# Kernel optimization log

Hardware: AMD Instinct MI355X
Metric: run time of the kernel (lower is better)

## Reference

```python
import jax, jax.numpy as jnp
import numpy as np

KH, KW, F = 2, 3, 32  # ConvLSTM kernel and filters


def _conv(x, w, padding):
    # x: [B,H,W,Cin], w: [kh,kw,Cin,Cout]
    return jax.lax.conv_general_dilated(
        x, w, (1, 1), padding, dimension_numbers=("NHWC", "HWIO", "NHWC"))


def _hard_sigmoid(x):
    # Keras hard_sigmoid: clip(0.2*x + 0.5, 0, 1)
    return jnp.clip(0.2 * x + 0.5, 0.0, 1.0)


def convlstm2d(x, W, U, b):
    # Keras ConvLSTM2D, padding='valid' on input conv, 'same' on recurrent conv,
    # activation=relu, recurrent_activation=hard_sigmoid, return_sequences=True.
    B, T, H, Wd, C = x.shape
    f = W.shape[-1] // 4
    Ho, Wo = H - KH + 1, Wd - KW + 1
    h0 = jnp.zeros((B, Ho, Wo, f), x.dtype)

    def step(carry, xt):
        h, c = carry
        z = _conv(xt, W, "VALID") + _conv(h, U, "SAME") + b
        zi, zf, zc, zo = jnp.split(z, 4, axis=-1)  # gate order i,f,c,o
        i = _hard_sigmoid(zi)
        fg = _hard_sigmoid(zf)
        c_new = fg * c + i * jax.nn.relu(zc)
        h_new = _hard_sigmoid(zo) * jax.nn.relu(c_new)
        return (h_new, c_new), h_new

    xs = jnp.moveaxis(x, 1, 0)  # [T,B,H,W,C]
    _, hs = jax.lax.scan(step, (h0, h0), xs)
    return jnp.moveaxis(hs, 0, 1)  # [B,T,Ho,Wo,F]


def maxpool3d(x):
    # MaxPooling3D pool_size=(1,2,2) over (T,H,W) of [B,T,H,W,C]
    return jax.lax.reduce_window(x, -jnp.inf, jax.lax.max,
                                 (1, 1, 2, 2, 1), (1, 1, 2, 2, 1), "VALID")


def setup_inputs() -> dict:
    key = jax.random.key(0)
    ks = jax.random.split(key, 12)
    s = 0.05
    B, T, H, Wd, C = 16, 12, 48, 48, 3
    x = jax.random.normal(ks[0], (B, T, H, Wd, C), jnp.float32)
    W1 = jax.random.normal(ks[1], (KH, KW, C, 4 * F), jnp.float32) * s
    U1 = jax.random.normal(ks[2], (KH, KW, F, 4 * F), jnp.float32) * s
    b1 = jnp.zeros((4 * F,), jnp.float32)
    W2 = jax.random.normal(ks[3], (KH, KW, F, 4 * F), jnp.float32) * s
    U2 = jax.random.normal(ks[4], (KH, KW, F, 4 * F), jnp.float32) * s
    b2 = jnp.zeros((4 * F,), jnp.float32)
    # after two convlstms: 48->47->46 (H), 48->46->44 (W); pool -> 23x22
    flat = T * 23 * 22 * F  # 194304
    Wd1 = jax.random.normal(ks[5], (flat, 10), jnp.float32) * 0.01
    bd1 = jnp.zeros((10,), jnp.float32)
    Wd2 = jax.random.normal(ks[6], (10, 1), jnp.float32) * 0.1
    bd2 = jnp.zeros((1,), jnp.float32)
    return {"x": x, "W1": W1, "U1": U1, "b1": b1, "W2": W2, "U2": U2,
            "b2": b2, "Wd1": Wd1, "bd1": bd1, "Wd2": Wd2, "bd2": bd2}


def reference(x, W1, U1, b1, W2, U2, b2, Wd1, bd1, Wd2, bd2):
    h1 = convlstm2d(x, W1, U1, b1)
    h2 = convlstm2d(h1, W2, U2, b2)
    p = maxpool3d(h2)            # dropout = identity at inference
    f = p.reshape(p.shape[0], -1)
    d1 = f @ Wd1 + bd1
    return d1 @ Wd2 + bd2        # [B,1]
```

## Files before the change

kernel.cpp:

```cpp
#include <hip/hip_runtime.h>
#include <math.h>

#define NB 16
#define TT 12
#define H1 47
#define W1D 46
#define H2 46
#define W2D 44

typedef short short8v __attribute__((ext_vector_type(8)));
typedef float floatx4 __attribute__((ext_vector_type(4)));

__device__ __forceinline__ short f2bf(float x) {
    unsigned u = __float_as_uint(x);
    u = (u + 0x7FFFu + ((u >> 16) & 1u)) >> 16;
    return (short)u;
}
__device__ __forceinline__ float bf2f(short s) {
    return __uint_as_float(((unsigned)(unsigned short)s) << 16);
}
__device__ __forceinline__ float hsig(float z) {
    return fminf(fmaxf(0.2f * z + 0.5f, 0.f), 1.f);
}

__global__ __launch_bounds__(256) void convert_x(const float* __restrict__ x,
                                                 short* __restrict__ xbf, int n) {
    int i = blockIdx.x * 256 + threadIdx.x;
    if (i < n) xbf[i] = f2bf(x[i]);
}

__global__ __launch_bounds__(256) void transform_w(
    const float* __restrict__ W1s, const float* __restrict__ U1s,
    const float* __restrict__ W2s, const float* __restrict__ U2s,
    short* __restrict__ Bt1, short* __restrict__ Bt2)
{
    int idx = blockIdx.x * 256 + threadIdx.x;
    int layer2 = idx >= 28672;
    int i = layer2 ? idx - 28672 : idx;
    int ci = i & 31, j = (i >> 5) & 15, g = (i >> 9) & 3, fh = (i >> 11) & 1, c = i >> 12;
    int col = g * 32 + fh * 16 + j;
    float v = 0.f;
    if (!layer2) {
        if (c == 0) {
            if (ci < 18) { int kk = ci / 3, cc = ci - kk * 3; v = W1s[(kk * 3 + cc) * 128 + col]; }
        } else {
            v = U1s[((c - 1) * 32 + ci) * 128 + col];
        }
    } else {
        if (c < 6) v = W2s[(c * 32 + ci) * 128 + col];
        else       v = U2s[((c - 6) * 32 + ci) * 128 + col];
    }
    (layer2 ? Bt2 : Bt1)[i] = f2bf(v);
}

template<int LAYER>
__device__ __forceinline__ void step_body(
    const short* __restrict__ xin,
    const short* __restrict__ hprev,
    const short* __restrict__ Bt,
    const float* __restrict__ bias,
    float* __restrict__ cstp,
    short* __restrict__ hnext,
    short* __restrict__ pool, int t2, int t1,
    int b, int y0, int x0, short* ldsrec, short* ldsaux)
{
    constexpr int Ho   = (LAYER == 1) ? H1 : H2;
    constexpr int Wo   = (LAYER == 1) ? W1D : W2D;
    constexpr int NCH  = (LAYER == 1) ? 7 : 12;
    constexpr int REC0 = (LAYER == 1) ? 1 : 6;
    constexpr int IBS  = (LAYER == 1) ? (TT * 48 * 48 * 3) : (H1 * W1D * 32);
    constexpr int HBS  = Ho * Wo * 32;

    const int tid = threadIdx.x;
    const int lane = tid & 63;
    const int fh = tid >> 6;
    const int tx = lane & 15, q = lane >> 4;
    const short8v z8 = (short8v)0;

    {
        const short* hb0 = hprev + b * HBS;
        for (int i = tid; i < 360; i += 128) {
            int p = i >> 2, c4 = i & 3;
            int row = p / 18, col = p - row * 18;
            int y = y0 + row, x = x0 + col - 1;
            short8v v = z8;
            if (y < Ho && (unsigned)x < (unsigned)Wo)
                v = *(const short8v*)(hb0 + (y * Wo + x) * 32 + c4 * 8);
            *(short8v*)&ldsrec[p * 40 + c4 * 8] = v;
        }
    }

    if (LAYER == 1) {
        const short* xb0 = xin + b * IBS + t1 * 6912;
        for (int i = tid; i < 64 * 32; i += 128) {
            int m = i >> 5, k = i & 31;
            short v = 0;
            if (k < 18) {
                int kk = k / 3, cc = k - kk * 3;
                int ky = (kk >= 3) ? 1 : 0, kx = kk - ky * 3;
                int ys = y0 + (m >> 4) + ky; if (ys > 47) ys = 47;
                int xs = x0 + (m & 15) + kx; if (xs > 47) xs = 47;
                v = xb0[(ys * 48 + xs) * 3 + cc];
            }
            ldsaux[m * 40 + k] = v;
        }
    } else {
        const short* ib0 = xin + b * IBS;
        for (int i = tid; i < 360; i += 128) {
            int p = i >> 2, c4 = i & 3;
            int row = p / 18, col = p - row * 18;
            int ys = y0 + row; if (ys > H1 - 1) ys = H1 - 1;
            int xs = x0 + col;
            short8v v = *(const short8v*)(ib0 + (ys * W1D + xs) * 32 + c4 * 8);
            *(short8v*)&ldsaux[p * 40 + c4 * 8] = v;
        }
    }
    __syncthreads();

    const short* Btl = Bt + fh * 2048 + tx * 32 + q * 8;
    floatx4 acc[4][4] = {};

#pragma unroll
    for (int c = 0; c < NCH; ++c) {
        short8v bf4[4], af[4];
#pragma unroll
        for (int g = 0; g < 4; ++g)
            bf4[g] = *(const short8v*)(Btl + c * 4096 + g * 512);

        if (LAYER == 1 && c == 0) {
#pragma unroll
            for (int a = 0; a < 4; ++a)
                af[a] = *(const short8v*)&ldsaux[(a * 16 + tx) * 40 + q * 8];
        } else if (LAYER == 2 && c < REC0) {
            int ky = (c >= 3) ? 1 : 0, kx = c - ky * 3;
#pragma unroll
            for (int a = 0; a < 4; ++a)
                af[a] = *(const short8v*)&ldsaux[(((a + ky) * 18 + tx + kx)) * 40 + q * 8];
        } else {
            int kk = c - REC0;
            int ky = (kk >= 3) ? 1 : 0, kx = kk - ky * 3;
#pragma unroll
            for (int a = 0; a < 4; ++a)
                af[a] = *(const short8v*)&ldsrec[(((a + ky) * 18 + tx + kx)) * 40 + q * 8];
        }
#pragma unroll
        for (int a = 0; a < 4; ++a)
#pragma unroll
            for (int g = 0; g < 4; ++g)
                acc[a][g] = __builtin_amdgcn_mfma_f32_16x16x32_bf16(af[a], bf4[g], acc[a][g], 0, 0, 0);
    }

    const int f = fh * 16 + tx;
    const float bi = bias[f], bfv = bias[32 + f], bcv = bias[64 + f], bov = bias[96 + f];
    float* cme = cstp + tid * 16;
    float hv[4][4];
#pragma unroll
    for (int a = 0; a < 4; ++a) {
        int y = y0 + a;
        bool yok = y < Ho;
        floatx4 cold = *(floatx4*)(cme + a * 4);
        floatx4 cnew;
#pragma unroll
        for (int r = 0; r < 4; ++r) {
            int xe = x0 + q * 4 + r;
            float ig = hsig(acc[a][0][r] + bi);
            float fg = hsig(acc[a][1][r] + bfv);
            float gg = fmaxf(acc[a][2][r] + bcv, 0.f);
            float og = hsig(acc[a][3][r] + bov);
            float cn = fg * cold[r] + ig * gg;
            cnew[r] = cn;
            float hn = 0.f;
            if (yok && xe < Wo) {
                short hb = f2bf(og * fmaxf(cn, 0.f));
                hnext[b * HBS + (y * Wo + xe) * 32 + f] = hb;
                hn = bf2f(hb);
            }
            hv[a][r] = hn;
        }
        *(floatx4*)(cme + a * 4) = cnew;
    }

    if (LAYER == 2) {
#pragma unroll
        for (int ap = 0; ap < 2; ++ap) {
            int py = y0 / 2 + ap;
#pragma unroll
            for (int rp = 0; rp < 2; ++rp) {
                int px = x0 / 2 + q * 2 + rp;
                if (py < 23 && px < 22) {
                    float m = fmaxf(fmaxf(hv[2 * ap][2 * rp],     hv[2 * ap][2 * rp + 1]),
                                    fmaxf(hv[2 * ap + 1][2 * rp], hv[2 * ap + 1][2 * rp + 1]));
                    pool[(size_t)b * 194304 + ((t2 * 23 + py) * 22 + px) * 32 + f] = f2bf(m);
                }
            }
        }
    }
}

__global__ __launch_bounds__(128) void fused_step(
    const short* __restrict__ xbf,
    const short* __restrict__ h1r, short* __restrict__ h1w,
    const short* __restrict__ h2r, short* __restrict__ h2w,
    const short* __restrict__ Bt1, const short* __restrict__ Bt2,
    const float* __restrict__ b1, const float* __restrict__ b2,
    float* __restrict__ c1, float* __restrict__ c2,
    short* __restrict__ pool, int t2, int t1, int do1, int do2)
{
    __shared__ short lds[7200];
    int gid  = blockIdx.x;
    int layer = gid & 1;
    int b     = (gid >> 1) & 15;
    int t36   = gid >> 5;
    int y0 = (t36 / 3) * 4;
    int x0 = (t36 % 3) * 16;

    if (layer == 0) {
        if (!do1) return;
        float* cstp = c1 + (size_t)(b * 36 + t36) * 2048;
        step_body<1>(xbf, h1r, Bt1, b1, cstp, h1w, nullptr, 0, t1,
                     b, y0, x0, lds, lds + 3600);
    } else {
        if (!do2) return;
        float* cstp = c2 + (size_t)(b * 36 + t36) * 2048;
        step_body<2>(h1r, h2r, Bt2, b2, cstp, h2w, pool, t2, 0,
                     b, y0, x0, lds, lds + 3600);
    }
}

__global__ __launch_bounds__(256) void gemv_kernel(
    const short* __restrict__ p, const float* __restrict__ Wd1, float* __restrict__ d1)
{
    int by = blockIdx.y;
    int k0 = blockIdx.x * 3036;
    float part[4][10];
#pragma unroll
    for (int bb = 0; bb < 4; bb++)
#pragma unroll
        for (int j = 0; j < 10; j++) part[bb][j] = 0.f;

    for (int k = k0 + threadIdx.x; k < k0 + 3036; k += 256) {
        const float* wr = Wd1 + (size_t)k * 10;
        float wv[10];
#pragma unroll
        for (int j = 0; j < 10; j++) wv[j] = wr[j];
#pragma unroll
        for (int bb = 0; bb < 4; bb++) {
            float m = bf2f(p[(size_t)(by * 4 + bb) * 194304 + k]);
#pragma unroll
            for (int j = 0; j < 10; j++) part[bb][j] = fmaf(m, wv[j], part[bb][j]);
        }
    }
    __shared__ float red[4][10][4];
    int lane = threadIdx.x & 63, wv2 = threadIdx.x >> 6;
#pragma unroll
    for (int bb = 0; bb < 4; bb++)
#pragma unroll
        for (int j = 0; j < 10; j++) {
            float v = part[bb][j];
            for (int off = 32; off > 0; off >>= 1) v += __shfl_down(v, off);
            if (lane == 0) red[bb][j][wv2] = v;
        }
    __syncthreads();
    if (threadIdx.x < 40) {
        int bb = threadIdx.x / 10, j = threadIdx.x % 10;
        float s = red[bb][j][0] + red[bb][j][1] + red[bb][j][2] + red[bb][j][3];
        atomicAdd(&d1[(by * 4 + bb) * 10 + j], s);
    }
}

__global__ void final_dense(const float* __restrict__ d1, const float* __restrict__ bd1,
                            const float* __restrict__ Wd2, const float* __restrict__ bd2,
                            float* __restrict__ out)
{
    int b = threadIdx.x;
    if (b < NB) {
        float s = bd2[0];
#pragma unroll
        for (int j = 0; j < 10; j++) s += (d1[b * 10 + j] + bd1[j]) * Wd2[j];
        out[b] = s;
    }
}

extern "C" void kernel_launch(void* const* d_in, const int* in_sizes, int n_in,
                              void* d_out, int out_size, void* d_ws, size_t ws_size,
                              hipStream_t stream)
{
    const float* x   = (const float*)d_in[0];
    const float* W1s = (const float*)d_in[1];
    const float* U1s = (const float*)d_in[2];
    const float* b1  = (const float*)d_in[3];
    const float* W2s = (const float*)d_in[4];
    const float* U2s = (const float*)d_in[5];
    const float* b2  = (const float*)d_in[6];
    const float* Wd1 = (const float*)d_in[7];
    const float* bd1 = (const float*)d_in[8];
    const float* Wd2 = (const float*)d_in[9];
    const float* bd2 = (const float*)d_in[10];
    float* out = (float*)d_out;

    const int H1N = NB * H1 * W1D * 32;
    const int H2N = NB * H2 * W2D * 32;
    const int SLF = 32, SLB = 8192;
    const int SPAN1 = SLF + H1N + SLB;
    const int SPAN2 = SLF + H2N + SLB;
    const int CPL   = 16 * 36 * 2048;

    short* Bt1 = (short*)d_ws;
    short* Bt2 = Bt1 + 28672;
    short* xbf = Bt2 + 49152;
    short* p   = xbf + 1327104;
    short* zr  = p + 3108864;
    short* h1a = zr + SLF;
    short* h1b = zr + SPAN1 + SLF;
    short* h2a = zr + 2 * SPAN1 + SLF;
    short* h2b = zr + 2 * SPAN1 + SPAN2 + SLF;
    float* c1  = (float*)(zr + 2 * SPAN1 + 2 * SPAN2);
    float* c2  = c1 + CPL;
    float* d1  = c2 + CPL;
    size_t zero_bytes = (size_t)(2 * SPAN1 + 2 * SPAN2) * 2 + (size_t)(2 * CPL + 160) * 4;

    hipMemsetAsync(zr, 0, zero_bytes, stream);
    convert_x<<<(1327104 + 255) / 256, 256, 0, stream>>>(x, xbf, 1327104);
    transform_w<<<304, 256, 0, stream>>>(W1s, U1s, W2s, U2s, Bt1, Bt2);

    for (int s = 0; s <= TT; s++) {
        short*       h1w = (s & 1) ? h1b : h1a;
        const short* h1r = (s & 1) ? h1a : h1b;
        short*       h2w = (s & 1) ? h2a : h2b;
        const short* h2r = (s & 1) ? h2b : h2a;
        fused_step<<<dim3(1152), 128, 0, stream>>>(
            xbf, h1r, h1w, h2r, h2w, Bt1, Bt2, b1, b2, c1, c2,
            p, s - 1, (s < TT ? s : 0), (int)(s < TT), (int)(s >= 1));
    }

    gemv_kernel<<<dim3(64, 4), 256, 0, stream>>>(p, Wd1, d1);
    final_dense<<<1, 64, 0, stream>>>(d1, bd1, Wd2, bd2, out);
}
```

Baseline: 301.5 us.

## Fuse two timesteps per launch using halo-extended tiles with recomputation

Each block now computes two consecutive ConvLSTM timesteps per layer in one launch. It first evaluates step t on a tile widened by a one-pixel halo (90 positions), keeps those h values in LDS, then uses them for step t+1 without a grid-wide sync. This halves the number of step launches (7 instead of 13) and avoids a global round trip for the intermediate hidden state. In exchange it recomputes halo work, with 6x4 accumulator tiles instead of 4x4, uses more LDS, and adds more hidden-state and cell-state buffers that are indexed by absolute position.

```diff
diff --git a/kernel.cpp b/kernel.cpp
--- a/kernel.cpp
+++ b/kernel.cpp
@@ -3,10 +3,11 @@
 
 #define NB 16
 #define TT 12
-#define H1 47
-#define W1D 46
-#define H2 46
-#define W2D 44
+#define H1B (47 * 46 * 32)
+#define H2B (46 * 44 * 32)
+#define H1SLOT (NB * H1B)
+#define H2SLOT (NB * H2B)
+#define XBSTRIDE (TT * 48 * 48 * 3)
 
 typedef short short8v __attribute__((ext_vector_type(8)));
 typedef float floatx4 __attribute__((ext_vector_type(4)));
@@ -53,134 +54,361 @@
     (layer2 ? Bt2 : Bt1)[i] = f2bf(v);
 }
 
-template<int LAYER>
-__device__ __forceinline__ void step_body(
-    const short* __restrict__ xin,
-    const short* __restrict__ hprev,
-    const short* __restrict__ Bt,
-    const float* __restrict__ bias,
-    float* __restrict__ cstp,
-    short* __restrict__ hnext,
-    short* __restrict__ pool, int t2, int t1,
-    int b, int y0, int x0, short* ldsrec, short* ldsaux)
-{
-    constexpr int Ho   = (LAYER == 1) ? H1 : H2;
-    constexpr int Wo   = (LAYER == 1) ? W1D : W2D;
-    constexpr int NCH  = (LAYER == 1) ? 7 : 12;
-    constexpr int REC0 = (LAYER == 1) ? 1 : 6;
-    constexpr int IBS  = (LAYER == 1) ? (TT * 48 * 48 * 3) : (H1 * W1D * 32);
-    constexpr int HBS  = Ho * Wo * 32;
+__device__ __forceinline__ void l1_block(
+    const short* __restrict__ xbf,
+    const short* __restrict__ h1rec,
+    short* __restrict__ h1wA,
+    short* __restrict__ h1wB,
+    const float* __restrict__ c1r, float* __restrict__ c1w,
+    const short* __restrict__ Bt, const float* __restrict__ bias,
+    int b, int y0, int x0, int tA, short* lds)
+{
+    short* REC = lds;
+    short* X1  = lds + 4800;
+    short* H   = lds + 4800;
+    short* X2  = lds;
+    float* CL  = (float*)(lds + 8640);
 
     const int tid = threadIdx.x;
     const int lane = tid & 63;
     const int fh = tid >> 6;
     const int tx = lane & 15, q = lane >> 4;
+    const int f = fh * 16 + tx;
     const short8v z8 = (short8v)0;
 
     {
-        const short* hb0 = hprev + b * HBS;
+        const short* hrb = h1rec + b * H1B;
+        for (int i = tid; i < 480; i += 128) {
+            int p = i >> 2, c4 = i & 3;
+            int row = p / 20, col = p - row * 20;
+            int y = y0 + row, x = x0 - 2 + col;
+            short8v v = z8;
+            if (y < 47 && (unsigned)x < 46u)
+                v = *(const short8v*)(hrb + (y * 46 + x) * 32 + c4 * 8);
+            *(short8v*)&REC[p * 40 + c4 * 8] = v;
+        }
+    }
+    {
+        const short* xb = xbf + b * XBSTRIDE + tA * 6912;
+        for (int i = tid; i < 3072; i += 128) {
+            int m = i >> 5, k2 = i & 31;
+            short v = 0;
+            if (k2 < 18 && m < 90) {
+                int kk = k2 / 3, cc = k2 - kk * 3;
+                int ky = (kk >= 3) ? 1 : 0, kx = kk - ky * 3;
+                int row = m / 18, col = m - row * 18;
+                int ys = y0 + row + ky; if (ys > 47) ys = 47;
+                int xs = x0 - 1 + col + kx; if (xs < 0) xs = 0; if (xs > 47) xs = 47;
+                v = xb[(ys * 48 + xs) * 3 + cc];
+            }
+            X1[m * 40 + k2] = v;
+        }
+    }
+    __syncthreads();
+
+    int baseA[6];
+#pragma unroll
+    for (int a = 0; a < 6; ++a) {
+        int p = a * 16 + tx;
+        baseA[a] = ((p / 18) * 20 + (p % 18)) * 40 + q * 8;
+    }
+    const short* Btl = Bt + fh * 2048 + tx * 32 + q * 8;
+
+    floatx4 acc[6][4] = {};
+#pragma unroll
+    for (int c = 0; c < 7; ++c) {
+        short8v bf4[4], af[6];
+#pragma unroll
+        for (int g = 0; g < 4; ++g)
+            bf4[g] = *(const short8v*)(Btl + c * 4096 + g * 512);
+        if (c == 0) {
+#pragma unroll
+            for (int a = 0; a < 6; ++a)
+                af[a] = *(const short8v*)&X1[(a * 16 + tx) * 40 + q * 8];
+        } else {
+            int kk = c - 1;
+            int ky = (kk >= 3) ? 1 : 0, kx = kk - ky * 3;
+            int off = (ky * 20 + kx) * 40;
+#pragma unroll
+            for (int a = 0; a < 6; ++a)
+                af[a] = *(const short8v*)&REC[baseA[a] + off];
+        }
+#pragma unroll
+        for (int a = 0; a < 6; ++a)
+#pragma unroll
+            for (int g = 0; g < 4; ++g)
+                acc[a][g] = __builtin_amdgcn_mfma_f32_16x16x32_bf16(af[a], bf4[g], acc[a][g], 0, 0, 0);
+    }
+    __syncthreads();
+
+    {
+        const short* xb2 = xbf + b * XBSTRIDE + (tA + 1) * 6912;
+        for (int i = tid; i < 2048; i += 128) {
+            int m = i >> 5, k2 = i & 31;
+            short v = 0;
+            if (k2 < 18) {
+                int kk = k2 / 3, cc = k2 - kk * 3;
+                int ky = (kk >= 3) ? 1 : 0, kx = kk - ky * 3;
+                int ys = y0 + (m >> 4) + ky; if (ys > 47) ys = 47;
+                int xs = x0 + (m & 15) + kx; if (xs > 47) xs = 47;
+                v = xb2[(ys * 48 + xs) * 3 + cc];
+            }
+            X2[m * 40 + k2] = v;
+        }
+    }
+
+    {
+        const float bi = bias[f], bf_ = bias[32 + f], bc_ = bias[64 + f], bo_ = bias[96 + f];
+        const float* crb = c1r + b * H1B;
+#pragma unroll
+        for (int a = 0; a < 6; ++a) {
+#pragma unroll
+            for (int r = 0; r < 4; ++r) {
+                int p = a * 16 + q * 4 + r;
+                int row = p / 18, col = p - row * 18;
+                int y = y0 + row, xe = x0 - 1 + col;
+                bool inb = (p < 90) && (y < 47) && ((unsigned)xe < 46u);
+                float cg = inb ? crb[(y * 46 + xe) * 32 + f] : 0.f;
+                float ig = hsig(acc[a][0][r] + bi);
+                float fg = hsig(acc[a][1][r] + bf_);
+                float gg = fmaxf(acc[a][2][r] + bc_, 0.f);
+                float og = hsig(acc[a][3][r] + bo_);
+                float cn = fg * cg + ig * gg;
+                short hb = inb ? f2bf(og * fmaxf(cn, 0.f)) : (short)0;
+                if (p < 90) H[p * 40 + f] = hb;
+                if (inb && row < 4 && col >= 1 && col <= 16) {
+                    h1wA[b * H1B + (y * 46 + xe) * 32 + f] = hb;
+                    CL[(row * 16 + (col - 1)) * 32 + f] = cn;
+                }
+            }
+        }
+    }
+    __syncthreads();
+
+    floatx4 ac2[4][4] = {};
+#pragma unroll
+    for (int c = 0; c < 7; ++c) {
+        short8v bf4[4], af[4];
+#pragma unroll
+        for (int g = 0; g < 4; ++g)
+            bf4[g] = *(const short8v*)(Btl + c * 4096 + g * 512);
+        if (c == 0) {
+#pragma unroll
+            for (int a = 0; a < 4; ++a)
+                af[a] = *(const short8v*)&X2[(a * 16 + tx) * 40 + q * 8];
+        } else {
+            int kk = c - 1;
+            int ky = (kk >= 3) ? 1 : 0, kx = kk - ky * 3;
+#pragma unroll
+            for (int a = 0; a < 4; ++a)
+                af[a] = *(const short8v*)&H[((a + ky) * 18 + tx + kx) * 40 + q * 8];
+        }
+#pragma unroll
+        for (int a = 0; a < 4; ++a)
+#pragma unroll
+            for (int g = 0; g < 4; ++g)
+                ac2[a][g] = __builtin_amdgcn_mfma_f32_16x16x32_bf16(af[a], bf4[g], ac2[a][g], 0, 0, 0);
+    }
+
+    {
+        const float bi = bias[f], bf_ = bias[32 + f], bc_ = bias[64 + f], bo_ = bias[96 + f];
+#pragma unroll
+        for (int a = 0; a < 4; ++a) {
+            int y = y0 + a;
+#pragma unroll
+            for (int r = 0; r < 4; ++r) {
+                int xe = x0 + q * 4 + r;
+                if (y < 47 && xe < 46) {
+                    float cg = CL[(a * 16 + q * 4 + r) * 32 + f];
+                    float ig = hsig(ac2[a][0][r] + bi);
+                    float fg = hsig(ac2[a][1][r] + bf_);
+                    float gg = fmaxf(ac2[a][2][r] + bc_, 0.f);
+                    float og = hsig(ac2[a][3][r] + bo_);
+                    float cn = fg * cg + ig * gg;
+                    int o = b * H1B + (y * 46 + xe) * 32 + f;
+                    c1w[o] = cn;
+                    h1wB[o] = f2bf(og * fmaxf(cn, 0.f));
+                }
+            }
+        }
+    }
+}
+
+__device__ __forceinline__ void l2_block(
+    const short* __restrict__ h1inA,
+    const short* __restrict__ h1inB,
+    const short* __restrict__ h2rec,
+    short* __restrict__ h2wB,
+    const float* __restrict__ c2r, float* __restrict__ c2w,
+    const short* __restrict__ Bt, const float* __restrict__ bias,
+    short* __restrict__ pool,
+    int b, int y0, int x0, int tA, short* lds)
+{
+    short* REC = lds;
+    short* IN1 = lds + 4800;
+    short* H   = lds + 4800;
+    short* IN2 = lds;
+    float* CL  = (float*)(lds + 9600);
+
+    const int tid = threadIdx.x;
+    const int lane = tid & 63;
+    const int fh = tid >> 6;
+    const int tx = lane & 15, q = lane >> 4;
+    const int f = fh * 16 + tx;
+    const short8v z8 = (short8v)0;
+
+    {
+        const short* hrb = h2rec + b * H2B;
+        for (int i = tid; i < 480; i += 128) {
+            int p = i >> 2, c4 = i & 3;
+            int row = p / 20, col = p - row * 20;
+            int y = y0 + row, x = x0 - 2 + col;
+            short8v v = z8;
+            if (y < 46 && (unsigned)x < 44u)
+                v = *(const short8v*)(hrb + (y * 44 + x) * 32 + c4 * 8);
+            *(short8v*)&REC[p * 40 + c4 * 8] = v;
+        }
+    }
+    {
+        const short* ib = h1inA + b * H1B;
+        for (int i = tid; i < 480; i += 128) {
+            int p = i >> 2, c4 = i & 3;
+            int row = p / 20, col = p - row * 20;
+            int ys = y0 + row; if (ys > 46) ys = 46;
+            int xs = x0 - 1 + col; if (xs < 0) xs = 0; if (xs > 45) xs = 45;
+            *(short8v*)&IN1[p * 40 + c4 * 8] =
+                *(const short8v*)(ib + (ys * 46 + xs) * 32 + c4 * 8);
+        }
+    }
+    __syncthreads();
+
+    int baseA[6];
+#pragma unroll
+    for (int a = 0; a < 6; ++a) {
+        int p = a * 16 + tx;
+        baseA[a] = ((p / 18) * 20 + (p % 18)) * 40 + q * 8;
+    }
+    const short* Btl = Bt + fh * 2048 + tx * 32 + q * 8;
+
+    floatx4 acc[6][4] = {};
+#pragma unroll
+    for (int c = 0; c < 12; ++c) {
+        short8v bf4[4], af[6];
+#pragma unroll
+        for (int g = 0; g < 4; ++g)
+            bf4[g] = *(const short8v*)(Btl + c * 4096 + g * 512);
+        int kk = (c < 6) ? c : (c - 6);
+        int ky = (kk >= 3) ? 1 : 0, kx = kk - ky * 3;
+        int off = (ky * 20 + kx) * 40;
+        const short* src = (c < 6) ? IN1 : REC;
+#pragma unroll
+        for (int a = 0; a < 6; ++a)
+            af[a] = *(const short8v*)&src[baseA[a] + off];
+#pragma unroll
+        for (int a = 0; a < 6; ++a)
+#pragma unroll
+            for (int g = 0; g < 4; ++g)
+                acc[a][g] = __builtin_amdgcn_mfma_f32_16x16x32_bf16(af[a], bf4[g], acc[a][g], 0, 0, 0);
+    }
+    __syncthreads();
+
+    {
+        const short* ib = h1inB + b * H1B;
         for (int i = tid; i < 360; i += 128) {
             int p = i >> 2, c4 = i & 3;
             int row = p / 18, col = p - row * 18;
-            int y = y0 + row, x = x0 + col - 1;
-            short8v v = z8;
-            if (y < Ho && (unsigned)x < (unsigned)Wo)
-                v = *(const short8v*)(hb0 + (y * Wo + x) * 32 + c4 * 8);
-            *(short8v*)&ldsrec[p * 40 + c4 * 8] = v;
-        }
-    }
-
-    if (LAYER == 1) {
-        const short* xb0 = xin + b * IBS + t1 * 6912;
-        for (int i = tid; i < 64 * 32; i += 128) {
-            int m = i >> 5, k = i & 31;
-            short v = 0;
-            if (k < 18) {
-                int kk = k / 3, cc = k - kk * 3;
-                int ky = (kk >= 3) ? 1 : 0, kx = kk - ky * 3;
-                int ys = y0 + (m >> 4) + ky; if (ys > 47) ys = 47;
-                int xs = x0 + (m & 15) + kx; if (xs > 47) xs = 47;
-                v = xb0[(ys * 48 + xs) * 3 + cc];
-            }
-            ldsaux[m * 40 + k] = v;
-        }
-    } else {
-        const short* ib0 = xin + b * IBS;
-        for (int i = tid; i < 360; i += 128) {
-            int p = i >> 2, c4 = i & 3;
-            int row = p / 18, col = p - row * 18;
-            int ys = y0 + row; if (ys > H1 - 1) ys = H1 - 1;
-            int xs = x0 + col;
-            short8v v = *(const short8v*)(ib0 + (ys * W1D + xs) * 32 + c4 * 8);
-            *(short8v*)&ldsaux[p * 40 + c4 * 8] = v;
-        }
-    }
-    __syncthreads();
-
-    const short* Btl = Bt + fh * 2048 + tx * 32 + q * 8;
-    floatx4 acc[4][4] = {};
-
-#pragma unroll
-    for (int c = 0; c < NCH; ++c) {
+            int ys = y0 + row; if (ys > 46) ys = 46;
+            int xs = x0 + col; if (xs > 45) xs = 45;
+            *(short8v*)&IN2[p * 40 + c4 * 8] =
+                *(const short8v*)(ib + (ys * 46 + xs) * 32 + c4 * 8);
+        }
+    }
+
+    {
+        const float bi = bias[f], bf_ = bias[32 + f], bc_ = bias[64 + f], bo_ = bias[96 + f];
+        const float* crb = c2r + b * H2B;
+#pragma unroll
+        for (int a = 0; a < 6; ++a) {
+#pragma unroll
+            for (int r = 0; r < 4; ++r) {
+                int p = a * 16 + q * 4 + r;
+                int row = p / 18, col = p - row * 18;
+                int y = y0 + row, xe = x0 - 1 + col;
+                bool inb = (p < 90) && (y < 46) && ((unsigned)xe < 44u);
+                float cg = inb ? crb[(y * 44 + xe) * 32 + f] : 0.f;
+                float ig = hsig(acc[a][0][r] + bi);
+                float fg = hsig(acc[a][1][r] + bf_);
+                float gg = fmaxf(acc[a][2][r] + bc_, 0.f);
+                float og = hsig(acc[a][3][r] + bo_);
+                float cn = fg * cg + ig * gg;
+                short hb = inb ? f2bf(og * fmaxf(cn, 0.f)) : (short)0;
+                if (p < 90) H[p * 40 + f] = hb;
+                if (inb && row < 4 && col >= 1 && col <= 16)
+                    CL[(row * 16 + (col - 1)) * 32 + f] = cn;
+            }
+        }
+    }
+    __syncthreads();
+
+    for (int i = tid; i < 512; i += 128) {
+        int f2 = i & 31, cell = i >> 5;
+        int ap = cell >> 3, j = cell & 7;
+        int py = y0 / 2 + ap, px = x0 / 2 + j;
+        if (py < 23 && px < 22) {
+            int p00 = (2 * ap) * 18 + (1 + 2 * j);
+            float m0 = bf2f(H[p00 * 40 + f2]),        m1 = bf2f(H[(p00 + 1) * 40 + f2]);
+            float m2 = bf2f(H[(p00 + 18) * 40 + f2]), m3 = bf2f(H[(p00 + 19) * 40 + f2]);
+            pool[(size_t)b * 194304 + ((tA * 23 + py) * 22 + px) * 32 + f2] =
+                f2bf(fmaxf(fmaxf(m0, m1), fmaxf(m2, m3)));
+        }
+    }
+
+    floatx4 ac2[4][4] = {};
+#pragma unroll
+    for (int c = 0; c < 12; ++c) {
         short8v bf4[4], af[4];
 #pragma unroll
         for (int g = 0; g < 4; ++g)
             bf4[g] = *(const short8v*)(Btl + c * 4096 + g * 512);
-
-        if (LAYER == 1 && c == 0) {
-#pragma unroll
-            for (int a = 0; a < 4; ++a)
-                af[a] = *(const short8v*)&ldsaux[(a * 16 + tx) * 40 + q * 8];
-        } else if (LAYER == 2 && c < REC0) {
-            int ky = (c >= 3) ? 1 : 0, kx = c - ky * 3;
-#pragma unroll
-            for (int a = 0; a < 4; ++a)
-                af[a] = *(const short8v*)&ldsaux[(((a + ky) * 18 + tx + kx)) * 40 + q * 8];
-        } else {
-            int kk = c - REC0;
-            int ky = (kk >= 3) ? 1 : 0, kx = kk - ky * 3;
-#pragma unroll
-            for (int a = 0; a < 4; ++a)
-                af[a] = *(const short8v*)&ldsrec[(((a + ky) * 18 + tx + kx)) * 40 + q * 8];
-        }
+        int kk = (c < 6) ? c : (c - 6);
+        int ky = (kk >= 3) ? 1 : 0, kx = kk - ky * 3;
+        const short* src = (c < 6) ? IN2 : H;
 #pragma unroll
         for (int a = 0; a < 4; ++a)
+            af[a] = *(const short8v*)&src[((a + ky) * 18 + tx + kx) * 40 + q * 8];
+#pragma unroll
+        for (int a = 0; a < 4; ++a)
 #pragma unroll
             for (int g = 0; g < 4; ++g)
-                acc[a][g] = __builtin_amdgcn_mfma_f32_16x16x32_bf16(af[a], bf4[g], acc[a][g], 0, 0, 0);
-    }
-
-    const int f = fh * 16 + tx;
-    const float bi = bias[f], bfv = bias[32 + f], bcv = bias[64 + f], bov = bias[96 + f];
-    float* cme = cstp + tid * 16;
-    float hv[4][4];
-#pragma unroll
-    for (int a = 0; a < 4; ++a) {
-        int y = y0 + a;
-        bool yok = y < Ho;
-        floatx4 cold = *(floatx4*)(cme + a * 4);
-        floatx4 cnew;
-#pragma unroll
-        for (int r = 0; r < 4; ++r) {
-            int xe = x0 + q * 4 + r;
-            float ig = hsig(acc[a][0][r] + bi);
-            float fg = hsig(acc[a][1][r] + bfv);
-            float gg = fmaxf(acc[a][2][r] + bcv, 0.f);
-            float og = hsig(acc[a][3][r] + bov);
-            float cn = fg * cold[r] + ig * gg;
-            cnew[r] = cn;
-            float hn = 0.f;
-            if (yok && xe < Wo) {
-                short hb = f2bf(og * fmaxf(cn, 0.f));
-                hnext[b * HBS + (y * Wo + xe) * 32 + f] = hb;
-                hn = bf2f(hb);
-            }
-            hv[a][r] = hn;
-        }
-        *(floatx4*)(cme + a * 4) = cnew;
-    }
-
-    if (LAYER == 2) {
+                ac2[a][g] = __builtin_amdgcn_mfma_f32_16x16x32_bf16(af[a], bf4[g], ac2[a][g], 0, 0, 0);
+    }
+
+    {
+        const float bi = bias[f], bf_ = bias[32 + f], bc_ = bias[64 + f], bo_ = bias[96 + f];
+        float hv[4][4];
+#pragma unroll
+        for (int a = 0; a < 4; ++a) {
+            int y = y0 + a;
+#pragma unroll
+            for (int r = 0; r < 4; ++r) {
+                int xe = x0 + q * 4 + r;
+                float hn = 0.f;
+                if (y < 46 && xe < 44) {
+                    float cg = CL[(a * 16 + q * 4 + r) * 32 + f];
+                    float ig = hsig(ac2[a][0][r] + bi);
+                    float fg = hsig(ac2[a][1][r] + bf_);
+                    float gg = fmaxf(ac2[a][2][r] + bc_, 0.f);
+                    float og = hsig(ac2[a][3][r] + bo_);
+                    float cn = fg * cg + ig * gg;
+                    int o = b * H2B + (y * 44 + xe) * 32 + f;
+                    c2w[o] = cn;
+                    short hb = f2bf(og * fmaxf(cn, 0.f));
+                    h2wB[o] = hb;
+                    hn = bf2f(hb);
+                }
+                hv[a][r] = hn;
+            }
+        }
 #pragma unroll
         for (int ap = 0; ap < 2; ++ap) {
             int py = y0 / 2 + ap;
@@ -190,40 +418,38 @@
                 if (py < 23 && px < 22) {
                     float m = fmaxf(fmaxf(hv[2 * ap][2 * rp],     hv[2 * ap][2 * rp + 1]),
                                     fmaxf(hv[2 * ap + 1][2 * rp], hv[2 * ap + 1][2 * rp + 1]));
-                    pool[(size_t)b * 194304 + ((t2 * 23 + py) * 22 + px) * 32 + f] = f2bf(m);
+                    pool[(size_t)b * 194304 + (((tA + 1) * 23 + py) * 22 + px) * 32 + f] = f2bf(m);
                 }
             }
         }
     }
 }
 
-__global__ __launch_bounds__(128) void fused_step(
+__global__ __launch_bounds__(128) void fused2(
     const short* __restrict__ xbf,
-    const short* __restrict__ h1r, short* __restrict__ h1w,
-    const short* __restrict__ h2r, short* __restrict__ h2w,
+    const short* __restrict__ h1rec, short* __restrict__ h1wA, short* __restrict__ h1wB,
+    const short* __restrict__ h1inA, const short* __restrict__ h1inB,
+    const short* __restrict__ h2rec, short* __restrict__ h2wB,
     const short* __restrict__ Bt1, const short* __restrict__ Bt2,
     const float* __restrict__ b1, const float* __restrict__ b2,
-    float* __restrict__ c1, float* __restrict__ c2,
-    short* __restrict__ pool, int t2, int t1, int do1, int do2)
-{
-    __shared__ short lds[7200];
-    int gid  = blockIdx.x;
+    const float* __restrict__ c1r, float* __restrict__ c1w,
+    const float* __restrict__ c2r, float* __restrict__ c2w,
+    short* __restrict__ pool, int tA1, int tA2)
+{
+    __shared__ short lds[13696];
+    int gid = blockIdx.x;
     int layer = gid & 1;
-    int b     = (gid >> 1) & 15;
-    int t36   = gid >> 5;
-    int y0 = (t36 / 3) * 4;
-    int x0 = (t36 % 3) * 16;
+    int b = (gid >> 1) & 15;
+    int tile = gid >> 5;
+    int y0 = (tile / 3) * 4;
+    int x0 = (tile % 3) * 16;
 
     if (layer == 0) {
-        if (!do1) return;
-        float* cstp = c1 + (size_t)(b * 36 + t36) * 2048;
-        step_body<1>(xbf, h1r, Bt1, b1, cstp, h1w, nullptr, 0, t1,
-                     b, y0, x0, lds, lds + 3600);
+        if (tA1 >= TT) return;
+        l1_block(xbf, h1rec, h1wA, h1wB, c1r, c1w, Bt1, b1, b, y0, x0, tA1, lds);
     } else {
-        if (!do2) return;
-        float* cstp = c2 + (size_t)(b * 36 + t36) * 2048;
-        step_body<2>(h1r, h2r, Bt2, b2, cstp, h2w, pool, t2, 0,
-                     b, y0, x0, lds, lds + 3600);
+        if (tA2 < 0) return;
+        l2_block(h1inA, h1inB, h2rec, h2wB, c2r, c2w, Bt2, b2, pool, b, y0, x0, tA2, lds);
     }
 }
 
@@ -264,7 +490,7 @@
     if (threadIdx.x < 40) {
         int bb = threadIdx.x / 10, j = threadIdx.x % 10;
         float s = red[bb][j][0] + red[bb][j][1] + red[bb][j][2] + red[bb][j][3];
-        atomicAdd(&d1[(by * 4 + bb) * 10 + j], s);
+        atomicAdd(&d1[(bb + 4 * 0 + by * 4) * 10 + j], s);
     }
 }
 
@@ -298,39 +524,43 @@
     const float* bd2 = (const float*)d_in[10];
     float* out = (float*)d_out;
 
-    const int H1N = NB * H1 * W1D * 32;
-    const int H2N = NB * H2 * W2D * 32;
-    const int SLF = 32, SLB = 8192;
-    const int SPAN1 = SLF + H1N + SLB;
-    const int SPAN2 = SLF + H2N + SLB;
-    const int CPL   = 16 * 36 * 2048;
-
     short* Bt1 = (short*)d_ws;
     short* Bt2 = Bt1 + 28672;
     short* xbf = Bt2 + 49152;
     short* p   = xbf + 1327104;
     short* zr  = p + 3108864;
-    short* h1a = zr + SLF;
-    short* h1b = zr + SPAN1 + SLF;
-    short* h2a = zr + 2 * SPAN1 + SLF;
-    short* h2b = zr + 2 * SPAN1 + SPAN2 + SLF;
-    float* c1  = (float*)(zr + 2 * SPAN1 + 2 * SPAN2);
-    float* c2  = c1 + CPL;
-    float* d1  = c2 + CPL;
-    size_t zero_bytes = (size_t)(2 * SPAN1 + 2 * SPAN2) * 2 + (size_t)(2 * CPL + 160) * 4;
+    short* h1s[4]; for (int i = 0; i < 4; i++) h1s[i] = zr + (size_t)i * H1SLOT;
+    short* h2base = zr + 4 * (size_t)H1SLOT;
+    short* h2s[3]; for (int i = 0; i < 3; i++) h2s[i] = h2base + (size_t)i * H2SLOT;
+    float* c1s[2]; c1s[0] = (float*)(h2base + 3 * (size_t)H2SLOT);
+    c1s[1] = c1s[0] + H1SLOT;
+    float* c2s[2]; c2s[0] = c1s[1] + H1SLOT;
+    c2s[1] = c2s[0] + H2SLOT;
+    float* d1 = c2s[1] + H2SLOT;
+    size_t zero_bytes = (size_t)(4 * H1SLOT + 3 * H2SLOT) * 2
+                      + (size_t)(2 * H1SLOT + 2 * H2SLOT + 160) * 4;
 
     hipMemsetAsync(zr, 0, zero_bytes, stream);
     convert_x<<<(1327104 + 255) / 256, 256, 0, stream>>>(x, xbf, 1327104);
     transform_w<<<304, 256, 0, stream>>>(W1s, U1s, W2s, U2s, Bt1, Bt2);
 
-    for (int s = 0; s <= TT; s++) {
-        short*       h1w = (s & 1) ? h1b : h1a;
-        const short* h1r = (s & 1) ? h1a : h1b;
-        short*       h2w = (s & 1) ? h2a : h2b;
-        const short* h2r = (s & 1) ? h2b : h2a;
-        fused_step<<<dim3(1152), 128, 0, stream>>>(
-            xbf, h1r, h1w, h2r, h2w, Bt1, Bt2, b1, b2, c1, c2,
-            p, s - 1, (s < TT ? s : 0), (int)(s < TT), (int)(s >= 1));
+    for (int k = 0; k < 7; ++k) {
+        int tA1 = 2 * k, tA2 = 2 * k - 2;
+        auto s3 = [](int t) { return ((t % 3) + 3) % 3; };
+        const short* h1rec = h1s[(2 * k - 1) & 3];
+        short* h1wA = h1s[(2 * k) & 3];
+        short* h1wB = h1s[(2 * k + 1) & 3];
+        const short* h1inA = h1s[(2 * k - 2) & 3];
+        const short* h1inB = h1s[(2 * k - 1) & 3];
+        const short* h2rec = h2s[s3(2 * k - 3)];
+        short* h2wB = h2s[s3(2 * k - 1)];
+        const float* c1r = c1s[(k + 1) & 1];
+        float* c1w = c1s[k & 1];
+        const float* c2r = c2s[(k + 1) & 1];
+        float* c2w = c2s[k & 1];
+        fused2<<<dim3(1152), 128, 0, stream>>>(
+            xbf, h1rec, h1wA, h1wB, h1inA, h1inB, h2rec, h2wB,
+            Bt1, Bt2, b1, b2, c1r, c1w, c2r, c2w, p, tA1, tA2);
     }
 
     gemv_kernel<<<dim3(64, 4), 256, 0, stream>>>(p, Wd1, d1);
```

Result: slower. 536.8 us (+78.1%).

## Drop state memset via first-step flags, regroup dense GEMV without atomics

Applied to the files above, without the earlier changes.

Removes the large memset of the hidden/cell state buffers. The first timestep of each layer now treats the previous h and c as zero through flags instead of reading zeroed memory. The dense GEMV now handles 8 batches per block, so each Wd1 row is loaded half as often, and it writes per-chunk partials that final_dense reduces instead of using atomics. It also adds an occupancy hint of 3 blocks per CU to the step kernel, which may cap register use and cause spills.

```diff
diff --git a/kernel.cpp b/kernel.cpp
--- a/kernel.cpp
+++ b/kernel.cpp
@@ -61,7 +61,7 @@
     const float* __restrict__ bias,
     float* __restrict__ cstp,
     short* __restrict__ hnext,
-    short* __restrict__ pool, int t2, int t1,
+    short* __restrict__ pool, int t2, int t1, int first,
     int b, int y0, int x0, short* ldsrec, short* ldsaux)
 {
     constexpr int Ho   = (LAYER == 1) ? H1 : H2;
@@ -84,7 +84,7 @@
             int row = p / 18, col = p - row * 18;
             int y = y0 + row, x = x0 + col - 1;
             short8v v = z8;
-            if (y < Ho && (unsigned)x < (unsigned)Wo)
+            if (!first && y < Ho && (unsigned)x < (unsigned)Wo)
                 v = *(const short8v*)(hb0 + (y * Wo + x) * 32 + c4 * 8);
             *(short8v*)&ldsrec[p * 40 + c4 * 8] = v;
         }
@@ -158,7 +158,9 @@
     for (int a = 0; a < 4; ++a) {
         int y = y0 + a;
         bool yok = y < Ho;
-        floatx4 cold = *(floatx4*)(cme + a * 4);
+        floatx4 cold;
+        if (first) { cold[0] = cold[1] = cold[2] = cold[3] = 0.f; }
+        else         cold = *(floatx4*)(cme + a * 4);
         floatx4 cnew;
 #pragma unroll
         for (int r = 0; r < 4; ++r) {
@@ -197,14 +199,15 @@
     }
 }
 
-__global__ __launch_bounds__(128) void fused_step(
+__global__ __launch_bounds__(128, 3) void fused_step(
     const short* __restrict__ xbf,
     const short* __restrict__ h1r, short* __restrict__ h1w,
     const short* __restrict__ h2r, short* __restrict__ h2w,
     const short* __restrict__ Bt1, const short* __restrict__ Bt2,
     const float* __restrict__ b1, const float* __restrict__ b2,
     float* __restrict__ c1, float* __restrict__ c2,
-    short* __restrict__ pool, int t2, int t1, int do1, int do2)
+    short* __restrict__ pool, int t2, int t1,
+    int do1, int do2, int first1, int first2)
 {
     __shared__ short lds[7200];
     int gid  = blockIdx.x;
@@ -217,24 +220,25 @@
     if (layer == 0) {
         if (!do1) return;
         float* cstp = c1 + (size_t)(b * 36 + t36) * 2048;
-        step_body<1>(xbf, h1r, Bt1, b1, cstp, h1w, nullptr, 0, t1,
+        step_body<1>(xbf, h1r, Bt1, b1, cstp, h1w, nullptr, 0, t1, first1,
                      b, y0, x0, lds, lds + 3600);
     } else {
         if (!do2) return;
         float* cstp = c2 + (size_t)(b * 36 + t36) * 2048;
-        step_body<2>(h1r, h2r, Bt2, b2, cstp, h2w, pool, t2, 0,
+        step_body<2>(h1r, h2r, Bt2, b2, cstp, h2w, pool, t2, 0, first2,
                      b, y0, x0, lds, lds + 3600);
     }
 }
 
 __global__ __launch_bounds__(256) void gemv_kernel(
-    const short* __restrict__ p, const float* __restrict__ Wd1, float* __restrict__ d1)
-{
-    int by = blockIdx.y;
-    int k0 = blockIdx.x * 3036;
-    float part[4][10];
-#pragma unroll
-    for (int bb = 0; bb < 4; bb++)
+    const short* __restrict__ p, const float* __restrict__ Wd1, float* __restrict__ d1p)
+{
+    int grp = blockIdx.y;
+    int kc = blockIdx.x;
+    int k0 = kc * 3036;
+    float part[8][10];
+#pragma unroll
+    for (int bb = 0; bb < 8; bb++)
 #pragma unroll
         for (int j = 0; j < 10; j++) part[bb][j] = 0.f;
 
@@ -244,16 +248,16 @@
 #pragma unroll
         for (int j = 0; j < 10; j++) wv[j] = wr[j];
 #pragma unroll
-        for (int bb = 0; bb < 4; bb++) {
-            float m = bf2f(p[(size_t)(by * 4 + bb) * 194304 + k]);
+        for (int bb = 0; bb < 8; bb++) {
+            float m = bf2f(p[(size_t)(grp * 8 + bb) * 194304 + k]);
 #pragma unroll
             for (int j = 0; j < 10; j++) part[bb][j] = fmaf(m, wv[j], part[bb][j]);
         }
     }
-    __shared__ float red[4][10][4];
+    __shared__ float red[8][10][4];
     int lane = threadIdx.x & 63, wv2 = threadIdx.x >> 6;
 #pragma unroll
-    for (int bb = 0; bb < 4; bb++)
+    for (int bb = 0; bb < 8; bb++)
 #pragma unroll
         for (int j = 0; j < 10; j++) {
             float v = part[bb][j];
@@ -261,23 +265,32 @@
             if (lane == 0) red[bb][j][wv2] = v;
         }
     __syncthreads();
-    if (threadIdx.x < 40) {
+    if (threadIdx.x < 80) {
         int bb = threadIdx.x / 10, j = threadIdx.x % 10;
-        float s = red[bb][j][0] + red[bb][j][1] + red[bb][j][2] + red[bb][j][3];
-        atomicAdd(&d1[(by * 4 + bb) * 10 + j], s);
-    }
-}
-
-__global__ void final_dense(const float* __restrict__ d1, const float* __restrict__ bd1,
+        d1p[(kc * 2 + grp) * 80 + bb * 10 + j] =
+            red[bb][j][0] + red[bb][j][1] + red[bb][j][2] + red[bb][j][3];
+    }
+}
+
+__global__ void final_dense(const float* __restrict__ d1p, const float* __restrict__ bd1,
                             const float* __restrict__ Wd2, const float* __restrict__ bd2,
                             float* __restrict__ out)
 {
-    int b = threadIdx.x;
-    if (b < NB) {
+    __shared__ float dj[16][10];
+    int tid = threadIdx.x;
+    if (tid < 160) {
+        int b = tid / 10, j = tid % 10, grp = b >> 3, bb = b & 7;
+        float s = 0.f;
+        for (int kc = 0; kc < 64; kc++)
+            s += d1p[(kc * 2 + grp) * 80 + bb * 10 + j];
+        dj[b][j] = s + bd1[j];
+    }
+    __syncthreads();
+    if (tid < NB) {
         float s = bd2[0];
 #pragma unroll
-        for (int j = 0; j < 10; j++) s += (d1[b * 10 + j] + bd1[j]) * Wd2[j];
-        out[b] = s;
+        for (int j = 0; j < 10; j++) s += dj[tid][j] * Wd2[j];
+        out[tid] = s;
     }
 }
 
@@ -309,17 +322,15 @@
     short* Bt2 = Bt1 + 28672;
     short* xbf = Bt2 + 49152;
     short* p   = xbf + 1327104;
-    short* zr  = p + 3108864;
-    short* h1a = zr + SLF;
-    short* h1b = zr + SPAN1 + SLF;
-    short* h2a = zr + 2 * SPAN1 + SLF;
-    short* h2b = zr + 2 * SPAN1 + SPAN2 + SLF;
-    float* c1  = (float*)(zr + 2 * SPAN1 + 2 * SPAN2);
+    short* hr  = p + 3108864;
+    short* h1a = hr + SLF;
+    short* h1b = hr + SPAN1 + SLF;
+    short* h2a = hr + 2 * SPAN1 + SLF;
+    short* h2b = hr + 2 * SPAN1 + SPAN2 + SLF;
+    float* c1  = (float*)(hr + 2 * SPAN1 + 2 * SPAN2);
     float* c2  = c1 + CPL;
-    float* d1  = c2 + CPL;
-    size_t zero_bytes = (size_t)(2 * SPAN1 + 2 * SPAN2) * 2 + (size_t)(2 * CPL + 160) * 4;
-
-    hipMemsetAsync(zr, 0, zero_bytes, stream);
+    float* d1p = c2 + CPL;
+
     convert_x<<<(1327104 + 255) / 256, 256, 0, stream>>>(x, xbf, 1327104);
     transform_w<<<304, 256, 0, stream>>>(W1s, U1s, W2s, U2s, Bt1, Bt2);
 
@@ -330,9 +341,10 @@
         const short* h2r = (s & 1) ? h2b : h2a;
         fused_step<<<dim3(1152), 128, 0, stream>>>(
             xbf, h1r, h1w, h2r, h2w, Bt1, Bt2, b1, b2, c1, c2,
-            p, s - 1, (s < TT ? s : 0), (int)(s < TT), (int)(s >= 1));
-    }
-
-    gemv_kernel<<<dim3(64, 4), 256, 0, stream>>>(p, Wd1, d1);
-    final_dense<<<1, 64, 0, stream>>>(d1, bd1, Wd2, bd2, out);
-}
+            p, s - 1, (s < TT ? s : 0),
+            (int)(s < TT), (int)(s >= 1), (int)(s == 0), (int)(s == 1));
+    }
+
+    gemv_kernel<<<dim3(64, 2), 256, 0, stream>>>(p, Wd1, d1p);
+    final_dense<<<1, 192, 0, stream>>>(d1p, bd1, Wd2, bd2, out);
+}
```

New measurement: 311.9 us. 3.4% more time.
